# Kernel tuning notes

Hardware: AMD Instinct MI355X
Metric: run time of the kernel (lower is better)

Reference implementation:

```python
import jax, jax.numpy as jnp
import numpy as np

B, T, H, DH = 4, 2048, 16, 128
D = H * DH            # inner_dim = 2048
F = 4096              # mlp_inner_dim
E = 8                 # num_expert_mlp
TOP_K = 2


def setup_inputs() -> dict:
    key = jax.random.key(0)
    ks = jax.random.split(key, 5)
    s_in = 1.0 / np.sqrt(D)
    s_f = 1.0 / np.sqrt(F)
    return {
        "stm": jax.random.normal(ks[0], (B, T, H, DH), dtype=jnp.float32),
        "gate_w": jax.random.normal(ks[1], (E, D), dtype=jnp.float32) * s_in,
        "w1": jax.random.normal(ks[2], (E, F, D), dtype=jnp.float32) * s_in,
        "w2": jax.random.normal(ks[3], (E, D, F), dtype=jnp.float32) * s_f,
        "w3": jax.random.normal(ks[4], (E, F, D), dtype=jnp.float32) * s_in,
    }


def reference(stm, gate_w, w1, w2, w3):
    b, t, h, dh = stm.shape
    d = h * dh
    x = stm.reshape(b * t, d)                                   # [N, D]
    logits = x @ gate_w.T                                       # [N, E]
    top_logit, top_idx = jax.lax.top_k(logits, TOP_K)           # [N, 2]
    gw = jax.nn.softmax(top_logit.astype(jnp.float32), axis=1).astype(x.dtype)
    out = jnp.zeros_like(x)
    n_expert = w1.shape[0]
    for e in range(n_expert):
        # combine weight for expert e per token (0 if not routed)
        we = jnp.sum(jnp.where(top_idx == e, gw, jnp.zeros_like(gw)), axis=1)  # [N]
        gate = jax.nn.silu(x @ w1[e].T)                          # [N, F]
        up = x @ w3[e].T                                         # [N, F]
        y = (gate * up) @ w2[e].T                                # [N, D]
        out = out + we[:, None] * y
    return out.reshape(b, t, h, dh)
```

## Files before the change

kernel.cpp:

```cpp
#include <hip/hip_runtime.h>
#include <hip/hip_bf16.h>
#include <stdint.h>

#define N_TOK 8192
#define DIM   2048
#define FDIM  4096
#define NEXP  8

#define XB_OFF   0ull
#define HB_OFF   33554432ull
#define WB1_OFF  176160768ull
#define WB3_OFF  243269632ull
#define META_OFF 310378496ull
#define CNT_OFF   (META_OFF)
#define EBASE_OFF (META_OFF + 64ull)
#define ELIST_OFF (META_OFF + 128ull)
#define EWTS_OFF  (ELIST_OFF + 262144ull)

typedef float f32x4 __attribute__((ext_vector_type(4)));
typedef short s16x8 __attribute__((ext_vector_type(8)));

__device__ __forceinline__ uint32_t pkbf(float a, float b) {
  uint32_t ua = __builtin_bit_cast(uint32_t, a) + 0x8000u;
  uint32_t ub = __builtin_bit_cast(uint32_t, b) + 0x8000u;
  return (ua >> 16) | (ub & 0xffff0000u);
}

__device__ __forceinline__ void gld16(const void* g, void* l) {
  __builtin_amdgcn_global_load_lds(
      (__attribute__((address_space(1))) void*)g,
      (__attribute__((address_space(3))) void*)l, 16, 0, 0);
}

__global__ void zero_out_k(float* out) {
  const size_t i = ((size_t)blockIdx.x * 256 + threadIdx.x) * 4;
  *(float4*)(out + i) = make_float4(0.f, 0.f, 0.f, 0.f);
}

__global__ void init_k(int* cnt) {
  if (threadIdx.x < NEXP) cnt[threadIdx.x] = 0;
}

__global__ void router_k(const float* __restrict__ x, const float* __restrict__ gw,
                         __hip_bfloat16* __restrict__ xb, int* __restrict__ cnt,
                         int* __restrict__ elist, float* __restrict__ ewts) {
  const int n = blockIdx.x;
  const int t = threadIdx.x;
  const float* xr = x + (size_t)n * DIM;
  const float4 v0 = *(const float4*)(xr + t * 8);
  const float4 v1 = *(const float4*)(xr + t * 8 + 4);
  uint4 u;
  u.x = pkbf(v0.x, v0.y); u.y = pkbf(v0.z, v0.w);
  u.z = pkbf(v1.x, v1.y); u.w = pkbf(v1.z, v1.w);
  *(uint4*)(xb + (size_t)n * DIM + t * 8) = u;

  float p[NEXP];
#pragma unroll
  for (int e = 0; e < NEXP; ++e) {
    const float* g = gw + e * DIM + t * 8;
    const float4 g0 = *(const float4*)g;
    const float4 g1 = *(const float4*)(g + 4);
    p[e] = v0.x * g0.x + v0.y * g0.y + v0.z * g0.z + v0.w * g0.w +
           v1.x * g1.x + v1.y * g1.y + v1.z * g1.z + v1.w * g1.w;
  }
#pragma unroll
  for (int off = 32; off >= 1; off >>= 1)
#pragma unroll
    for (int e = 0; e < NEXP; ++e) p[e] += __shfl_xor(p[e], off, 64);

  __shared__ float red[4][NEXP];
  const int lane = t & 63, wv = t >> 6;
  if (lane == 0) {
#pragma unroll
    for (int e = 0; e < NEXP; ++e) red[wv][e] = p[e];
  }
  __syncthreads();
  if (t == 0) {
    float l0 = -1e30f, l1 = -1e30f;
    int e0 = 0, e1 = 0;
#pragma unroll
    for (int e = 0; e < NEXP; ++e) {
      float v = red[0][e] + red[1][e] + red[2][e] + red[3][e];
      if (v > l0) { l1 = l0; e1 = e0; l0 = v; e0 = e; }
      else if (v > l1) { l1 = v; e1 = e; }
    }
    const float ed = expf(l1 - l0);
    const float inv = 1.f / (1.f + ed);
    int s0 = atomicAdd(cnt + e0, 1);
    elist[e0 * N_TOK + s0] = n;
    ewts[e0 * N_TOK + s0] = inv;
    int s1 = atomicAdd(cnt + e1, 1);
    elist[e1 * N_TOK + s1] = (int)((uint32_t)n | 0x80000000u);
    ewts[e1 * N_TOK + s1] = ed * inv;
  }
}

__global__ void scan_k(const int* __restrict__ cnt, int* __restrict__ ebase) {
  if (threadIdx.x == 0 && blockIdx.x == 0) {
    int b = 0;
    for (int e = 0; e < NEXP; ++e) { ebase[e] = b; b += (cnt[e] + 127) & ~127; }
  }
}

__global__ void convW_k(const float* __restrict__ src, __hip_bfloat16* __restrict__ dst,
                        int r0, int nrh, int rtot, int kd) {
  const int cpr = kd / 8;
  const int total = NEXP * nrh * cpr;
  for (int i = blockIdx.x * blockDim.x + threadIdx.x; i < total;
       i += gridDim.x * blockDim.x) {
    const int e = i / (nrh * cpr);
    const int rem = i - e * nrh * cpr;
    const int lr = rem / cpr;
    const int c = rem - lr * cpr;
    const float* s = src + ((size_t)e * rtot + r0 + lr) * (size_t)kd + c * 8;
    const float4 a = *(const float4*)s;
    const float4 b = *(const float4*)(s + 4);
    uint4 u;
    u.x = pkbf(a.x, a.y); u.y = pkbf(a.z, a.w);
    u.z = pkbf(b.x, b.y); u.w = pkbf(b.z, b.w);
    *(uint4*)(dst + ((size_t)e * nrh + lr) * (size_t)kd + c * 8) = u;
  }
}

__global__ __launch_bounds__(256, 2) void moe_up_k(
    const __hip_bfloat16* __restrict__ xb, const __hip_bfloat16* __restrict__ w1b,
    const __hip_bfloat16* __restrict__ w3b, __hip_bfloat16* __restrict__ hb,
    const int* __restrict__ cnt, const int* __restrict__ ebase,
    const int* __restrict__ elist, int noff) {
  const int e = blockIdx.z;
  const int count = cnt[e];
  const int mt = blockIdx.y;
  if (mt * 128 >= count) return;
  const int bn0 = blockIdx.x * 128;
  const int ncol0 = noff + bn0;

  __shared__ char lds[49152];
  const int t = threadIdx.x;
  const int lane = t & 63, wv = t >> 6;
  const int wr = wv >> 1, wc = wv & 1;
  const int* lst = elist + e * N_TOK;
  const size_t hrow0 = (size_t)ebase[e] + (size_t)mt * 128;

  const int r0 = t >> 2;
  const int ks = (t & 3) ^ ((r0 >> 1) & 3);
  size_t sA[2], sB1[2];
  int ldsO[2];
#pragma unroll
  for (int i = 0; i < 2; ++i) {
    const int r = r0 + i * 64;
    int idx = mt * 128 + r;
    if (idx >= count) idx = 0;
    const size_t tok = (size_t)(lst[idx] & 0x7fffffff);
    sA[i] = tok * DIM + ks * 8;
    sB1[i] = ((size_t)e * 2048 + bn0 + r) * DIM + ks * 8;
    ldsO[i] = i * 4096 + wv * 1024;
  }

  const int fr = lane & 15;
  const int swzc = ((lane >> 4) ^ ((fr >> 1) & 3)) << 4;
  const int aoff = (wr * 64 + fr) * 64 + swzc;
  const int boff = (wc * 64 + fr) * 64 + swzc;

  f32x4 accG[4][4], accU[4][4];
#pragma unroll
  for (int mi = 0; mi < 4; ++mi)
#pragma unroll
    for (int ni = 0; ni < 4; ++ni) {
      accG[mi][ni] = {0.f, 0.f, 0.f, 0.f};
      accU[mi][ni] = {0.f, 0.f, 0.f, 0.f};
    }

  auto stage = [&](int k0, int b) {
#pragma unroll
    for (int i = 0; i < 2; ++i)
      gld16(xb + sA[i] + k0, lds + b * 8192 + ldsO[i]);
#pragma unroll
    for (int i = 0; i < 2; ++i)
      gld16(w1b + sB1[i] + k0, lds + 16384 + b * 8192 + ldsO[i]);
#pragma unroll
    for (int i = 0; i < 2; ++i)
      gld16(w3b + sB1[i] + k0, lds + 32768 + b * 8192 + ldsO[i]);
  };

  stage(0, 0);
  __syncthreads();

  int b = 0;
  for (int kt = 0; kt < DIM / 32; ++kt) {
    const int nk = (kt + 1) * 32;
    if (nk < DIM) stage(nk, b ^ 1);
    s16x8 af[4], b1f[4], b3f[4];
#pragma unroll
    for (int mi = 0; mi < 4; ++mi)
      af[mi] = *(const s16x8*)(lds + b * 8192 + aoff + mi * 1024);
#pragma unroll
    for (int ni = 0; ni < 4; ++ni) {
      b1f[ni] = *(const s16x8*)(lds + 16384 + b * 8192 + boff + ni * 1024);
      b3f[ni] = *(const s16x8*)(lds + 32768 + b * 8192 + boff + ni * 1024);
    }
#pragma unroll
    for (int mi = 0; mi < 4; ++mi)
#pragma unroll
      for (int ni = 0; ni < 4; ++ni) {
        accG[mi][ni] = __builtin_amdgcn_mfma_f32_16x16x32_bf16(
            af[mi], b1f[ni], accG[mi][ni], 0, 0, 0);
        accU[mi][ni] = __builtin_amdgcn_mfma_f32_16x16x32_bf16(
            af[mi], b3f[ni], accU[mi][ni], 0, 0, 0);
      }
    __syncthreads();
    b ^= 1;
  }

  const int erow = (lane >> 4) * 4;
  const int ecol = lane & 15;
#pragma unroll
  for (int mi = 0; mi < 4; ++mi)
#pragma unroll
    for (int ni = 0; ni < 4; ++ni) {
      const size_t cb = ncol0 + wc * 64 + ni * 16 + ecol;
#pragma unroll
      for (int j = 0; j < 4; ++j) {
        const size_t r = hrow0 + wr * 64 + mi * 16 + erow + j;
        const float g = accG[mi][ni][j];
        const float uu = accU[mi][ni][j];
        const float h = g / (1.f + __expf(-g)) * uu;
        hb[r * FDIM + cb] = __float2bfloat16(h);
      }
    }
}

__global__ __launch_bounds__(256, 2) void moe_down_k(
    const __hip_bfloat16* __restrict__ hb, const __hip_bfloat16* __restrict__ w2b,
    float* __restrict__ out, const int* __restrict__ cnt,
    const int* __restrict__ ebase, const int* __restrict__ elist,
    const float* __restrict__ ewts) {
  constexpr int NT = FDIM / 32;
  const int e = blockIdx.x;
  const int count = cnt[e];
  const int mt = blockIdx.y;
  if (mt * 128 >= count) return;
  const int bn0 = blockIdx.z * 256;

  __shared__ char lds[73728];
  const int t = threadIdx.x;
  const int lane = t & 63, wv = t >> 6;
  const int wr = wv >> 1, wc = wv & 1;
  const int* lst = elist + e * N_TOK;
  const size_t hrow0 = (size_t)ebase[e] + (size_t)mt * 128;

  const int r0 = t >> 2;
  const int ks = (t & 3) ^ ((r0 >> 1) & 3);
  size_t sA[2], sB[2];
  int ldsO[2];
#pragma unroll
  for (int i = 0; i < 2; ++i) {
    const int r = r0 + i * 64;
    sA[i] = (hrow0 + r) * (size_t)FDIM + ks * 8;
    sB[i] = ((size_t)e * 2048 + bn0 + r) * (size_t)FDIM + ks * 8;
    ldsO[i] = i * 4096 + wv * 1024;
  }
  const size_t sBp = 128 * (size_t)FDIM;

  const int fr = lane & 15;
  const int swzc = ((lane >> 4) ^ ((fr >> 1) & 3)) << 4;
  const int aoff = (wr * 64 + fr) * 64 + swzc;
  const int boff = (wc * 64 + fr) * 64 + swzc;

  f32x4 accP[2][4][4];
#pragma unroll
  for (int p = 0; p < 2; ++p)
#pragma unroll
    for (int mi = 0; mi < 4; ++mi)
#pragma unroll
      for (int ni = 0; ni < 4; ++ni) accP[p][mi][ni] = {0.f, 0.f, 0.f, 0.f};

  auto stage = [&](int kt, int b) {
    const int k0 = kt * 32;
    char* base = lds + b * 24576;
#pragma unroll
    for (int i = 0; i < 2; ++i)
      gld16(hb + sA[i] + k0, base + ldsO[i]);
#pragma unroll
    for (int i = 0; i < 2; ++i)
      gld16(w2b + sB[i] + k0, base + 8192 + ldsO[i]);
#pragma unroll
    for (int i = 0; i < 2; ++i)
      gld16(w2b + sB[i] + sBp + k0, base + 16384 + ldsO[i]);
  };

  stage(0, 0);
  stage(1, 1);
  asm volatile("s_waitcnt vmcnt(6)" ::: "memory");
  __builtin_amdgcn_sched_barrier(0);
  __builtin_amdgcn_s_barrier();
  __builtin_amdgcn_sched_barrier(0);

  int bR = 0, bS = 2;
#pragma unroll 3
  for (int kt = 0; kt < NT; ++kt) {
    const int t2 = (kt + 2 < NT) ? kt + 2 : NT - 1;
    stage(t2, bS);
    char* base = lds + bR * 24576;
    s16x8 af[4], b0f[4], b1f[4];
#pragma unroll
    for (int mi = 0; mi < 4; ++mi)
      af[mi] = *(const s16x8*)(base + aoff + mi * 1024);
#pragma unroll
    for (int ni = 0; ni < 4; ++ni) {
      b0f[ni] = *(const s16x8*)(base + 8192 + boff + ni * 1024);
      b1f[ni] = *(const s16x8*)(base + 16384 + boff + ni * 1024);
    }
#pragma unroll
    for (int mi = 0; mi < 4; ++mi)
#pragma unroll
      for (int ni = 0; ni < 4; ++ni) {
        accP[0][mi][ni] = __builtin_amdgcn_mfma_f32_16x16x32_bf16(
            af[mi], b0f[ni], accP[0][mi][ni], 0, 0, 0);
        accP[1][mi][ni] = __builtin_amdgcn_mfma_f32_16x16x32_bf16(
            af[mi], b1f[ni], accP[1][mi][ni], 0, 0, 0);
      }
    asm volatile("s_waitcnt vmcnt(6)" ::: "memory");
    __builtin_amdgcn_sched_barrier(0);
    __builtin_amdgcn_s_barrier();
    __builtin_amdgcn_sched_barrier(0);
    bR = (bR == 2) ? 0 : bR + 1;
    bS = (bS == 2) ? 0 : bS + 1;
  }

  const int erow = (lane >> 4) * 4;
  const int ecol = lane & 15;
#pragma unroll
  for (int mi = 0; mi < 4; ++mi)
#pragma unroll
    for (int j = 0; j < 4; ++j) {
      const int i = mt * 128 + wr * 64 + mi * 16 + erow + j;
      if (i < count) {
        const uint32_t info = (uint32_t)lst[i];
        const int tok = (int)(info & 0x7fffffffu);
        const float wt = ewts[e * N_TOK + i];
        float* prow = out + (size_t)tok * DIM;
#pragma unroll
        for (int p = 0; p < 2; ++p)
#pragma unroll
          for (int ni = 0; ni < 4; ++ni) {
            const int cb = bn0 + p * 128 + wc * 64 + ni * 16 + ecol;
            atomicAdd(prow + cb, wt * accP[p][mi][ni][j]);
          }
      }
    }
}

extern "C" void kernel_launch(void* const* d_in, const int* in_sizes, int n_in,
                              void* d_out, int out_size, void* d_ws, size_t ws_size,
                              hipStream_t stream) {
  const float* stm = (const float*)d_in[0];
  const float* gw = (const float*)d_in[1];
  const float* w1 = (const float*)d_in[2];
  const float* w2 = (const float*)d_in[3];
  const float* w3 = (const float*)d_in[4];
  float* out = (float*)d_out;
  char* ws = (char*)d_ws;

  __hip_bfloat16* xb = (__hip_bfloat16*)(ws + XB_OFF);
  __hip_bfloat16* hb = (__hip_bfloat16*)(ws + HB_OFF);
  __hip_bfloat16* wb1 = (__hip_bfloat16*)(ws + WB1_OFF);
  __hip_bfloat16* wb3 = (__hip_bfloat16*)(ws + WB3_OFF);
  __hip_bfloat16* w2full = (__hip_bfloat16*)(ws + WB1_OFF);
  int* cnt = (int*)(ws + CNT_OFF);
  int* ebase = (int*)(ws + EBASE_OFF);
  int* elist = (int*)(ws + ELIST_OFF);
  float* ewts = (float*)(ws + EWTS_OFF);

  init_k<<<1, 64, 0, stream>>>(cnt);
  router_k<<<N_TOK, 256, 0, stream>>>(stm, gw, xb, cnt, elist, ewts);
  scan_k<<<1, 64, 0, stream>>>(cnt, ebase);
  zero_out_k<<<N_TOK * DIM / 1024, 256, 0, stream>>>(out);

  const dim3 gUp(16, 64, 8);
  const dim3 gDn(8, 64, 8);

  convW_k<<<2048, 256, 0, stream>>>(w1, wb1, 0, 2048, FDIM, DIM);
  convW_k<<<2048, 256, 0, stream>>>(w3, wb3, 0, 2048, FDIM, DIM);
  moe_up_k<<<gUp, 256, 0, stream>>>(xb, wb1, wb3, hb, cnt, ebase, elist, 0);
  convW_k<<<2048, 256, 0, stream>>>(w1, wb1, 2048, 2048, FDIM, DIM);
  convW_k<<<2048, 256, 0, stream>>>(w3, wb3, 2048, 2048, FDIM, DIM);
  moe_up_k<<<gUp, 256, 0, stream>>>(xb, wb1, wb3, hb, cnt, ebase, elist, 2048);

  convW_k<<<4096, 256, 0, stream>>>(w2, w2full, 0, 2048, DIM, FDIM);
  moe_down_k<<<gDn, 256, 0, stream>>>(hb, w2full, out, cnt, ebase, elist, ewts);
}
```

Before: 1.384 ms.

## Triple-buffer LDS in MoE up-projection with partial vmcnt waits

Moves the fused gate/up GEMM kernel from double to triple buffering in LDS, so two K-tiles are in flight while one is computed. The full __syncthreads is replaced by an s_waitcnt vmcnt(6) plus a raw s_barrier, so only the oldest stage's loads have to land before each step. LDS per block grows from 48KB to 72KB, which may reduce how many blocks fit per CU. The last iterations redundantly re-stage the final tile to keep the wait count uniform.

```diff
diff --git a/kernel.cpp b/kernel.cpp
--- a/kernel.cpp
+++ b/kernel.cpp
@@ -127,6 +127,7 @@
     const __hip_bfloat16* __restrict__ w3b, __hip_bfloat16* __restrict__ hb,
     const int* __restrict__ cnt, const int* __restrict__ ebase,
     const int* __restrict__ elist, int noff) {
+  constexpr int NT = DIM / 32;
   const int e = blockIdx.z;
   const int count = cnt[e];
   const int mt = blockIdx.y;
@@ -134,7 +135,7 @@
   const int bn0 = blockIdx.x * 128;
   const int ncol0 = noff + bn0;
 
-  __shared__ char lds[49152];
+  __shared__ char lds[73728];
   const int t = threadIdx.x;
   const int lane = t & 63, wv = t >> 6;
   const int wr = wv >> 1, wc = wv & 1;
@@ -170,33 +171,41 @@
       accU[mi][ni] = {0.f, 0.f, 0.f, 0.f};
     }
 
-  auto stage = [&](int k0, int b) {
-#pragma unroll
-    for (int i = 0; i < 2; ++i)
-      gld16(xb + sA[i] + k0, lds + b * 8192 + ldsO[i]);
-#pragma unroll
-    for (int i = 0; i < 2; ++i)
-      gld16(w1b + sB1[i] + k0, lds + 16384 + b * 8192 + ldsO[i]);
-#pragma unroll
-    for (int i = 0; i < 2; ++i)
-      gld16(w3b + sB1[i] + k0, lds + 32768 + b * 8192 + ldsO[i]);
+  auto stage = [&](int kt, int b) {
+    const int k0 = kt * 32;
+    char* base = lds + b * 24576;
+#pragma unroll
+    for (int i = 0; i < 2; ++i)
+      gld16(xb + sA[i] + k0, base + ldsO[i]);
+#pragma unroll
+    for (int i = 0; i < 2; ++i)
+      gld16(w1b + sB1[i] + k0, base + 8192 + ldsO[i]);
+#pragma unroll
+    for (int i = 0; i < 2; ++i)
+      gld16(w3b + sB1[i] + k0, base + 16384 + ldsO[i]);
   };
 
   stage(0, 0);
-  __syncthreads();
-
-  int b = 0;
-  for (int kt = 0; kt < DIM / 32; ++kt) {
-    const int nk = (kt + 1) * 32;
-    if (nk < DIM) stage(nk, b ^ 1);
+  stage(1, 1);
+  asm volatile("s_waitcnt vmcnt(6)" ::: "memory");
+  __builtin_amdgcn_sched_barrier(0);
+  __builtin_amdgcn_s_barrier();
+  __builtin_amdgcn_sched_barrier(0);
+
+  int bR = 0, bS = 2;
+#pragma unroll 3
+  for (int kt = 0; kt < NT; ++kt) {
+    const int t2 = (kt + 2 < NT) ? kt + 2 : NT - 1;
+    stage(t2, bS);
+    char* base = lds + bR * 24576;
     s16x8 af[4], b1f[4], b3f[4];
 #pragma unroll
     for (int mi = 0; mi < 4; ++mi)
-      af[mi] = *(const s16x8*)(lds + b * 8192 + aoff + mi * 1024);
+      af[mi] = *(const s16x8*)(base + aoff + mi * 1024);
 #pragma unroll
     for (int ni = 0; ni < 4; ++ni) {
-      b1f[ni] = *(const s16x8*)(lds + 16384 + b * 8192 + boff + ni * 1024);
-      b3f[ni] = *(const s16x8*)(lds + 32768 + b * 8192 + boff + ni * 1024);
+      b1f[ni] = *(const s16x8*)(base + 8192 + boff + ni * 1024);
+      b3f[ni] = *(const s16x8*)(base + 16384 + boff + ni * 1024);
     }
 #pragma unroll
     for (int mi = 0; mi < 4; ++mi)
@@ -207,8 +216,12 @@
         accU[mi][ni] = __builtin_amdgcn_mfma_f32_16x16x32_bf16(
             af[mi], b3f[ni], accU[mi][ni], 0, 0, 0);
       }
-    __syncthreads();
-    b ^= 1;
+    asm volatile("s_waitcnt vmcnt(6)" ::: "memory");
+    __builtin_amdgcn_sched_barrier(0);
+    __builtin_amdgcn_s_barrier();
+    __builtin_amdgcn_sched_barrier(0);
+    bR = (bR == 2) ? 0 : bR + 1;
+    bS = (bS == 2) ? 0 : bS + 1;
   }
 
   const int erow = (lane >> 4) * 4;
```

Result: faster. 1.349 ms (-2.6%).
